# Optimization experiments

Hardware: AMD Instinct MI355X
Metric: run time of the kernel (lower is better)

Reference implementation:

```python
import jax, jax.numpy as jnp
import numpy as np

B, H, W, C = 16, 64, 64, 192
NUM_HEADS, KEY_DIM, KS = 8, 32, 3


def setup_inputs() -> dict:
    key = jax.random.key(0)
    ks = jax.random.split(key, 9)
    Ck = C + 2  # key/value input dim: patches concat 2 dist channels
    def w(k, shape, fan_in):
        return jax.random.normal(k, shape, jnp.float32) / np.float32(np.sqrt(fan_in))
    return {
        "x": jax.random.normal(ks[0], (B, H, W, C), jnp.float32),
        "Wq": w(ks[1], (C, NUM_HEADS, KEY_DIM), C),
        "bq": jnp.zeros((NUM_HEADS, KEY_DIM), jnp.float32),
        "Wk": w(ks[2], (Ck, NUM_HEADS, KEY_DIM), Ck),
        "bk": jnp.zeros((NUM_HEADS, KEY_DIM), jnp.float32),
        "Wv": w(ks[3], (Ck, NUM_HEADS, KEY_DIM), Ck),
        "bv": jnp.zeros((NUM_HEADS, KEY_DIM), jnp.float32),
        "Wo": w(ks[4], (NUM_HEADS, KEY_DIM, C), NUM_HEADS * KEY_DIM),
        "bo": jnp.zeros((C,), jnp.float32),
    }


def _local_window_kv(x, ks):
    # tf.image.extract_patches SAME (zero pad) -> [B,H,W,ks*ks,C]
    pad = ks // 2
    xp = jnp.pad(x, ((0, 0), (pad, pad), (pad, pad), (0, 0)))
    b, h, w, c = x.shape
    patches = jnp.stack(
        [xp[:, i:i + h, j:j + w, :] for i in range(ks) for j in range(ks)], axis=3
    )  # [B,H,W,ks*ks,C], row-major over window like extract_patches
    # relative distances: tf.meshgrid default 'xy', concat (dists[0], dists[1])
    r = jnp.arange(ks, dtype=x.dtype) - ks // 2
    dx, dy = jnp.meshgrid(r, r)  # 'xy' indexing, matches tf.meshgrid default
    dists = jnp.stack([dx, dy], axis=-1).reshape(ks * ks, 2)  # [9,2]
    dists = jnp.broadcast_to(dists, (b, h, w, ks * ks, 2))
    return jnp.concatenate([patches, dists], axis=-1)  # [B,H,W,9,C+2]


def reference(x, Wq, bq, Wk, bk, Wv, bv, Wo, bo):
    kv_in = _local_window_kv(x, KS)  # [B,H,W,9,C+2]
    # keras MultiHeadAttention projections
    q = jnp.einsum('bxyc,chd->bxyhd', x, Wq) + bq           # [B,H,W,h,d] (q_len=1)
    k = jnp.einsum('bxykc,chd->bxykhd', kv_in, Wk) + bk     # [B,H,W,9,h,d]
    v = jnp.einsum('bxykc,chd->bxykhd', kv_in, Wv) + bv
    scale = np.float32(1.0 / np.sqrt(KEY_DIM))
    scores = jnp.einsum('bxyhd,bxykhd->bxyhk', q, k) * scale  # [B,H,W,h,9]
    attn = jax.nn.softmax(scores, axis=-1)
    o = jnp.einsum('bxyhk,bxykhd->bxyhd', attn, v)
    return jnp.einsum('bxyhd,hdc->bxyc', o, Wo) + bo          # [B,H,W,C]
```

## Files before the change

kernel.cpp:

```cpp
#include <hip/hip_runtime.h>
#include <hip/hip_bf16.h>


typedef __bf16 bf16x8_t __attribute__((ext_vector_type(8)));
typedef float f32x4_t __attribute__((ext_vector_type(4)));

#define SCALE 0.17677669529663687f
#define QSTRIDE 864
#define ZROW 65536

static __device__ __forceinline__ unsigned short bfbits(float f) {
    return __builtin_bit_cast(unsigned short, __float2bfloat16(f));
}
static __device__ __forceinline__ float bf2f(unsigned short u) {
    return __bfloat162float(__builtin_bit_cast(__hip_bfloat16, u));
}
static __device__ __forceinline__ float lo16f(unsigned int u) {
    return __builtin_bit_cast(float, u << 16);
}
static __device__ __forceinline__ float hi16f(unsigned int u) {
    return __builtin_bit_cast(float, u & 0xffff0000u);
}

static __device__ __forceinline__ void gload_lds16(const void* g, void* l) {
    __builtin_amdgcn_global_load_lds((const __attribute__((address_space(1))) void*)g,
                                     (__attribute__((address_space(3))) void*)l, 16, 0, 0);
}

__global__ void k_convert_x(const float* __restrict__ x, ushort4* __restrict__ xb, int n4) {
    int i = blockIdx.x * blockDim.x + threadIdx.x;
    const int stride = gridDim.x * blockDim.x;
    const float4* x4 = reinterpret_cast<const float4*>(x);
    for (; i < n4; i += stride) {
        float4 v = x4[i];
        ushort4 o;
        o.x = bfbits(v.x); o.y = bfbits(v.y); o.z = bfbits(v.z); o.w = bfbits(v.w);
        xb[i] = o;
    }
}

__global__ void k_pack(const float* __restrict__ Wq, const float* __restrict__ Wk,
                       const float* __restrict__ Wv, const float* __restrict__ Wo,
                       const float* __restrict__ bq, const float* __restrict__ bk,
                       const float* __restrict__ bv,
                       __hip_bfloat16* __restrict__ WqkvT, __hip_bfloat16* __restrict__ WoT,
                       float* __restrict__ qkvBias, float* __restrict__ wvTab,
                       __hip_bfloat16* __restrict__ QKV) {
    const int idx = blockIdx.x * blockDim.x + threadIdx.x;
    const int T0 = 896 * 192;
    const int T1 = T0 + 192 * 256;
    const int T2 = T1 + 896;
    const int T3 = T2 + 768;
    const int T4 = T3 + QSTRIDE;
    if (idx < T0) {
        const int m = idx / 192, k = idx % 192;
        float v = 0.f;
        if (m < 256) {
            v = Wq[k * 256 + m] * SCALE;
        } else if (m < 768) {
            const int j = m - 256, g = j >> 3, r = j & 7;
            const int d = 4 * g + (r & 3);
            v = (r < 4) ? Wk[k * 256 + d] : Wv[k * 256 + d];
        } else if (m < 864) {
            const int j = m - 768, h = j / 12, n = j % 12;
            if (n < 9) {
                const float dj = (float)(n % 3 - 1), di = (float)(n / 3 - 1);
                float acc = 0.f;
                for (int d = 0; d < 32; ++d) {
                    const int c = h * 32 + d;
                    const float bkv = dj * Wk[192 * 256 + c] + di * Wk[193 * 256 + c] + bk[c];
                    acc += Wq[k * 256 + c] * bkv;
                }
                v = acc * SCALE;
            }
        }
        WqkvT[m * 192 + k] = __float2bfloat16(v);
    } else if (idx < T1) {
        const int j = idx - T0;
        const int c = j >> 8, hd = j & 255;
        WoT[j] = __float2bfloat16(Wo[hd * 192 + c]);
    } else if (idx < T2) {
        const int col = idx - T1;
        float v = 0.f;
        if (col < 256) v = bq[col] * SCALE;
        else if (col >= 768 && col < 864) {
            const int j = col - 768, h = j / 12, n = j % 12;
            if (n < 9) {
                const float dj = (float)(n % 3 - 1), di = (float)(n / 3 - 1);
                float acc = 0.f;
                for (int d = 0; d < 32; ++d) {
                    const int c = h * 32 + d;
                    const float bkv = dj * Wk[192 * 256 + c] + di * Wk[193 * 256 + c] + bk[c];
                    acc += bq[c] * bkv;
                }
                v = acc * SCALE;
            }
        }
        qkvBias[col] = v;
    } else if (idx < T3) {
        const int j = idx - T2;
        const int t = j >> 8, m = j & 255;
        float v;
        if (t == 0)      v = Wv[192 * 256 + m];
        else if (t == 1) v = Wv[193 * 256 + m];
        else             v = bv[m];
        wvTab[j] = v;
    } else if (idx < T4) {
        const int j = idx - T3;
        QKV[(size_t)ZROW * QSTRIDE + j] = __float2bfloat16(0.f);
    }
}

template<int BM, int BN, int WRN, int WCN, int KDIM, int NOUT, int NBX, bool OUTF32, bool BIAS>
__global__ __launch_bounds__(256) void k_gemm_lds(const __hip_bfloat16* __restrict__ A,
                          const __hip_bfloat16* __restrict__ BT,
                          void* __restrict__ Cout,
                          const float* __restrict__ bias, int ldc) {
    constexpr int WTR = BM / WRN;
    constexpr int WTC = BN / WCN;
    constexpr int FR = WTR / 16;
    constexpr int FC = WTC / 16;
    constexpr int NK = KDIM / 64;
    __shared__ __hip_bfloat16 sA[BM * 64];
    __shared__ __hip_bfloat16 sB[BN * 64];
    const int bid = blockIdx.x;
    const int s = (bid & 7) * ((int)gridDim.x >> 3) + (bid >> 3);
    const int by = s / NBX, bx = s - by * NBX;
    const int tid = threadIdx.x;
    const int wave = tid >> 6, lane = tid & 63;
    const int wr = wave / WCN, wc = wave % WCN;
    const long rowBase = (long)by * BM;
    const long colBase = (long)bx * BN;
    const int lr = lane & 15, lk = lane >> 4;
    const int srow = lane >> 3;
    const int scol = (lane & 7) * 8;

    f32x4_t acc[FR][FC] = {};
    for (int t = 0; t < NK; ++t) {
        const int k0 = t * 64;
        #pragma unroll
        for (int r = 0; r < BM / 32; ++r) {
            const int row0 = r * 32 + wave * 8;
            gload_lds16(A + (rowBase + row0 + srow) * KDIM + k0 + scol, sA + row0 * 64);
        }
        #pragma unroll
        for (int r = 0; r < BN / 32; ++r) {
            const int row0 = r * 32 + wave * 8;
            gload_lds16(BT + (colBase + row0 + srow) * KDIM + k0 + scol, sB + row0 * 64);
        }
        __syncthreads();
        #pragma unroll
        for (int kk = 0; kk < 64; kk += 32) {
            bf16x8_t a[FR], b[FC];
            #pragma unroll
            for (int fr = 0; fr < FR; ++fr)
                a[fr] = *reinterpret_cast<const bf16x8_t*>(sA + (wr * WTR + fr * 16 + lr) * 64 + kk + lk * 8);
            #pragma unroll
            for (int fc = 0; fc < FC; ++fc)
                b[fc] = *reinterpret_cast<const bf16x8_t*>(sB + (wc * WTC + fc * 16 + lr) * 64 + kk + lk * 8);
            #pragma unroll
            for (int fr = 0; fr < FR; ++fr) {
                #pragma unroll
                for (int fc = 0; fc < FC; ++fc)
                    acc[fr][fc] = __builtin_amdgcn_mfma_f32_16x16x32_bf16(a[fr], b[fc], acc[fr][fc], 0, 0, 0);
            }
        }
        __syncthreads();
    }
    const int rowSub = (lane >> 4) * 4;
    const int colSub = lane & 15;
    #pragma unroll
    for (int fr = 0; fr < FR; ++fr) {
        #pragma unroll
        for (int fc = 0; fc < FC; ++fc) {
            const long col = colBase + wc * WTC + fc * 16 + colSub;
            if (col >= NOUT) continue;
            float bvv = BIAS ? bias[col] : 0.f;
            #pragma unroll
            for (int r = 0; r < 4; ++r) {
                const long row = rowBase + wr * WTR + fr * 16 + rowSub + r;
                float v = acc[fr][fc][r] + bvv;
                if constexpr (OUTF32) ((float*)Cout)[row * ldc + col] = v;
                else ((__hip_bfloat16*)Cout)[row * ldc + col] = __float2bfloat16(v);
            }
        }
    }
}

__global__ __launch_bounds__(256) void k_attn(const __hip_bfloat16* __restrict__ QKV,
                       const float* __restrict__ wvTab,
                       __hip_bfloat16* __restrict__ O) {
    const int wave = threadIdx.x >> 6;
    const int lane = threadIdx.x & 63;
    const int bid = blockIdx.x;
    const int sblk = (bid & 7) * 2048 + (bid >> 3);
    const int p = sblk * 4 + wave;
    const int y = (p >> 6) & 63;
    const int xq = p & 63;
    const int h = lane >> 3, dg = lane & 7;
    const int idx = h * 32 + dg * 4;
    const __hip_bfloat16* rowQ = QKV + (size_t)p * QSTRIDE;

    const ushort4 qu = *reinterpret_cast<const ushort4*>(rowQ + idx);
    const float q0 = bf2f(qu.x), q1 = bf2f(qu.y), q2 = bf2f(qu.z), q3 = bf2f(qu.w);

    const ushort4 qba = *reinterpret_cast<const ushort4*>(rowQ + 768 + 12 * h);
    const ushort4 qbb = *reinterpret_cast<const ushort4*>(rowQ + 772 + 12 * h);
    const unsigned short qbc = *reinterpret_cast<const unsigned short*>(rowQ + 776 + 12 * h);
    float qb[9] = { bf2f(qba.x), bf2f(qba.y), bf2f(qba.z), bf2f(qba.w),
                    bf2f(qbb.x), bf2f(qbb.y), bf2f(qbb.z), bf2f(qbb.w), bf2f(qbc) };

    const char* baseQ = reinterpret_cast<const char*>(QKV);
    const long rowByte = (long)p * (QSTRIDE * 2);
    const int laneOff = 512 + 128 * h + 16 * dg;
    uint4 kv[9];
    #pragma unroll
    for (int n = 0; n < 9; ++n) {
        const int di = n / 3 - 1, dj = n % 3 - 1;
        const int ny = y + di, nx = xq + dj;
        const bool inb = ((unsigned)ny < 64u) & ((unsigned)nx < 64u);
        const long off = inb ? rowByte + (long)((di * 64 + dj) * (QSTRIDE * 2))
                             : (long)ZROW * (QSTRIDE * 2);
        kv[n] = *reinterpret_cast<const uint4*>(baseQ + off + laneOff);
    }

    float sc[9];
    #pragma unroll
    for (int n = 0; n < 9; ++n) {
        const float k0 = lo16f(kv[n].x), k1 = hi16f(kv[n].x);
        const float k2 = lo16f(kv[n].y), k3 = hi16f(kv[n].y);
        float ss = fmaf(q0, k0, fmaf(q1, k1, fmaf(q2, k2, q3 * k3)));
        ss += __shfl_xor(ss, 1);
        ss += __shfl_xor(ss, 2);
        ss += __shfl_xor(ss, 4);
        sc[n] = ss + qb[n];
    }
    float mx = sc[0];
    #pragma unroll
    for (int n = 1; n < 9; ++n) mx = fmaxf(mx, sc[n]);
    float sum = 0.f;
    #pragma unroll
    for (int n = 0; n < 9; ++n) { sc[n] = __expf(sc[n] - mx); sum += sc[n]; }
    const float inv = 1.0f / sum;
    const float Ej = (sc[2] + sc[5] + sc[8]) - (sc[0] + sc[3] + sc[6]);
    const float Ei = (sc[6] + sc[7] + sc[8]) - (sc[0] + sc[1] + sc[2]);

    float o0 = 0.f, o1 = 0.f, o2 = 0.f, o3 = 0.f;
    #pragma unroll
    for (int n = 0; n < 9; ++n) {
        o0 = fmaf(sc[n], lo16f(kv[n].z), o0);
        o1 = fmaf(sc[n], hi16f(kv[n].z), o1);
        o2 = fmaf(sc[n], lo16f(kv[n].w), o2);
        o3 = fmaf(sc[n], hi16f(kv[n].w), o3);
    }
    const float4 w0 = *reinterpret_cast<const float4*>(wvTab + idx);
    const float4 w1 = *reinterpret_cast<const float4*>(wvTab + 256 + idx);
    const float4 w2 = *reinterpret_cast<const float4*>(wvTab + 512 + idx);
    o0 = fmaf(Ej, w0.x, fmaf(Ei, w1.x, o0)) * inv + w2.x;
    o1 = fmaf(Ej, w0.y, fmaf(Ei, w1.y, o1)) * inv + w2.y;
    o2 = fmaf(Ej, w0.z, fmaf(Ei, w1.z, o2)) * inv + w2.z;
    o3 = fmaf(Ej, w0.w, fmaf(Ei, w1.w, o3)) * inv + w2.w;

    ushort4 ov;
    ov.x = bfbits(o0); ov.y = bfbits(o1); ov.z = bfbits(o2); ov.w = bfbits(o3);
    *reinterpret_cast<ushort4*>(O + (size_t)p * 256 + idx) = ov;
}

extern "C" void kernel_launch(void* const* d_in, const int* in_sizes, int n_in,
                              void* d_out, int out_size, void* d_ws, size_t ws_size,
                              hipStream_t stream) {
    (void)in_sizes; (void)n_in; (void)out_size; (void)ws_size;
    const float* x  = (const float*)d_in[0];
    const float* Wq = (const float*)d_in[1];
    const float* bq = (const float*)d_in[2];
    const float* Wk = (const float*)d_in[3];
    const float* bk = (const float*)d_in[4];
    const float* Wv = (const float*)d_in[5];
    const float* bv = (const float*)d_in[6];
    const float* Wo = (const float*)d_in[7];
    const float* bo = (const float*)d_in[8];

    char* ws = (char*)d_ws;
    __hip_bfloat16* xb    = (__hip_bfloat16*)(ws + 0);
    __hip_bfloat16* O     = (__hip_bfloat16*)(ws + 0);
    __hip_bfloat16* QKV   = (__hip_bfloat16*)(ws + 33554432);
    __hip_bfloat16* WqkvT = (__hip_bfloat16*)(ws + 146802368);
    __hip_bfloat16* WoT   = (__hip_bfloat16*)(ws + 147146432);
    float* qkvBias        = (float*)(ws + 147244736);
    float* wvTab          = (float*)(ws + 147248320);

    k_convert_x<<<4096, 256, 0, stream>>>(x, (ushort4*)xb, 12582912 / 4);
    k_pack<<<874, 256, 0, stream>>>(Wq, Wk, Wv, Wo, bq, bk, bv, WqkvT, WoT, qkvBias, wvTab, QKV);
    k_gemm_lds<128, 128, 2, 2, 192, 864, 7, false, true>
        <<<3584, 256, 0, stream>>>(xb, WqkvT, (void*)QKV, qkvBias, QSTRIDE);
    k_attn<<<16384, 256, 0, stream>>>(QKV, wvTab, O);
    k_gemm_lds<128, 64, 2, 2, 256, 192, 3, true, true>
        <<<1536, 256, 0, stream>>>(O, WoT, d_out, bo, 192);
}
```

Baseline: 120.1 us.

## Keep full B tile resident in LDS and read A directly from global

The GEMM kernel now stages the whole K-extent of the weight tile into LDS once, with an XOR swizzle to avoid bank conflicts, and drops the per-k-step A staging. Each wave reads its A fragments directly from global memory into registers. This removes the per-iteration barriers and LDS round-trips for A. In exchange, A reuse across the waves that share rows now depends on the cache, global A loads are uncoalesced 16-byte fragment reads, and the larger LDS footprint may lower occupancy.

```diff
diff --git a/kernel.cpp b/kernel.cpp
--- a/kernel.cpp
+++ b/kernel.cpp
@@ -112,7 +112,7 @@
 }
 
 template<int BM, int BN, int WRN, int WCN, int KDIM, int NOUT, int NBX, bool OUTF32, bool BIAS>
-__global__ __launch_bounds__(256) void k_gemm_lds(const __hip_bfloat16* __restrict__ A,
+__global__ __launch_bounds__(256) void k_gemm_bres(const __hip_bfloat16* __restrict__ A,
                           const __hip_bfloat16* __restrict__ BT,
                           void* __restrict__ Cout,
                           const float* __restrict__ bias, int ldc) {
@@ -120,53 +120,49 @@
     constexpr int WTC = BN / WCN;
     constexpr int FR = WTR / 16;
     constexpr int FC = WTC / 16;
-    constexpr int NK = KDIM / 64;
-    __shared__ __hip_bfloat16 sA[BM * 64];
-    __shared__ __hip_bfloat16 sB[BN * 64];
+    constexpr int CH = KDIM / 8;
+    constexpr int NSTG = BN * CH / 256;
+    __shared__ __hip_bfloat16 sB[BN * KDIM];
     const int bid = blockIdx.x;
     const int s = (bid & 7) * ((int)gridDim.x >> 3) + (bid >> 3);
     const int by = s / NBX, bx = s - by * NBX;
     const int tid = threadIdx.x;
     const int wave = tid >> 6, lane = tid & 63;
     const int wr = wave / WCN, wc = wave % WCN;
-    const long rowBase = (long)by * BM;
+    const long rowBase = (long)by * BM + wr * WTR;
     const long colBase = (long)bx * BN;
     const int lr = lane & 15, lk = lane >> 4;
-    const int srow = lane >> 3;
-    const int scol = (lane & 7) * 8;
+
+    #pragma unroll
+    for (int r = 0; r < NSTG; ++r) {
+        const int g = r * 256 + tid;
+        const int row = g / CH, p = g % CH;
+        const int l = p ^ (row & 7);
+        gload_lds16(BT + (colBase + row) * KDIM + l * 8, sB + g * 8);
+    }
+    __syncthreads();
 
     f32x4_t acc[FR][FC] = {};
-    for (int t = 0; t < NK; ++t) {
-        const int k0 = t * 64;
-        #pragma unroll
-        for (int r = 0; r < BM / 32; ++r) {
-            const int row0 = r * 32 + wave * 8;
-            gload_lds16(A + (rowBase + row0 + srow) * KDIM + k0 + scol, sA + row0 * 64);
-        }
-        #pragma unroll
-        for (int r = 0; r < BN / 32; ++r) {
-            const int row0 = r * 32 + wave * 8;
-            gload_lds16(BT + (colBase + row0 + srow) * KDIM + k0 + scol, sB + row0 * 64);
-        }
-        __syncthreads();
-        #pragma unroll
-        for (int kk = 0; kk < 64; kk += 32) {
-            bf16x8_t a[FR], b[FC];
-            #pragma unroll
-            for (int fr = 0; fr < FR; ++fr)
-                a[fr] = *reinterpret_cast<const bf16x8_t*>(sA + (wr * WTR + fr * 16 + lr) * 64 + kk + lk * 8);
+    #pragma unroll
+    for (int k0 = 0; k0 < KDIM; k0 += 32) {
+        bf16x8_t a[FR], b[FC];
+        #pragma unroll
+        for (int fr = 0; fr < FR; ++fr)
+            a[fr] = *reinterpret_cast<const bf16x8_t*>(A + (rowBase + fr * 16 + lr) * KDIM + k0 + lk * 8);
+        #pragma unroll
+        for (int fc = 0; fc < FC; ++fc) {
+            const int col = wc * WTC + fc * 16 + lr;
+            const int p = ((k0 / 8) + lk) ^ (col & 7);
+            b[fc] = *reinterpret_cast<const bf16x8_t*>(sB + col * KDIM + p * 8);
+        }
+        #pragma unroll
+        for (int fr = 0; fr < FR; ++fr) {
             #pragma unroll
             for (int fc = 0; fc < FC; ++fc)
-                b[fc] = *reinterpret_cast<const bf16x8_t*>(sB + (wc * WTC + fc * 16 + lr) * 64 + kk + lk * 8);
-            #pragma unroll
-            for (int fr = 0; fr < FR; ++fr) {
-                #pragma unroll
-                for (int fc = 0; fc < FC; ++fc)
-                    acc[fr][fc] = __builtin_amdgcn_mfma_f32_16x16x32_bf16(a[fr], b[fc], acc[fr][fc], 0, 0, 0);
-            }
-        }
-        __syncthreads();
-    }
+                acc[fr][fc] = __builtin_amdgcn_mfma_f32_16x16x32_bf16(a[fr], b[fc], acc[fr][fc], 0, 0, 0);
+        }
+    }
+
     const int rowSub = (lane >> 4) * 4;
     const int colSub = lane & 15;
     #pragma unroll
@@ -178,7 +174,7 @@
             float bvv = BIAS ? bias[col] : 0.f;
             #pragma unroll
             for (int r = 0; r < 4; ++r) {
-                const long row = rowBase + wr * WTR + fr * 16 + rowSub + r;
+                const long row = rowBase + fr * 16 + rowSub + r;
                 float v = acc[fr][fc][r] + bvv;
                 if constexpr (OUTF32) ((float*)Cout)[row * ldc + col] = v;
                 else ((__hip_bfloat16*)Cout)[row * ldc + col] = __float2bfloat16(v);
@@ -291,9 +287,9 @@
 
     k_convert_x<<<4096, 256, 0, stream>>>(x, (ushort4*)xb, 12582912 / 4);
     k_pack<<<874, 256, 0, stream>>>(Wq, Wk, Wv, Wo, bq, bk, bv, WqkvT, WoT, qkvBias, wvTab, QKV);
-    k_gemm_lds<128, 128, 2, 2, 192, 864, 7, false, true>
+    k_gemm_bres<128, 128, 2, 2, 192, 864, 7, false, true>
         <<<3584, 256, 0, stream>>>(xb, WqkvT, (void*)QKV, qkvBias, QSTRIDE);
     k_attn<<<16384, 256, 0, stream>>>(QKV, wvTab, O);
-    k_gemm_lds<128, 64, 2, 2, 256, 192, 3, true, true>
+    k_gemm_bres<128, 64, 2, 2, 256, 192, 3, true, true>
         <<<1536, 256, 0, stream>>>(O, WoT, d_out, bo, 192);
 }
```

Result: slower. 154.3 us (+28.4%).

## Fuse fp32-to-bf16 conversion into QKV GEMM and pipeline with swizzled LDS

Applied to the files above, without the earlier changes.

The standalone x conversion kernel is removed. The QKV GEMM now loads fp32 x through registers, converts it to bf16 and writes it into LDS itself. The GEMM also gains a double-buffered B tile (prefetched via global_load_lds for the next k-step) and XOR-swizzled LDS layouts for both A and B to avoid bank conflicts. The intent is to remove a full read/write pass over x and to overlap loads with MFMA work, at the cost of more registers and extra barriers for the register-staged A path. Each QKV block now reads fp32 A directly, so x is re-read in its 4-byte form once per column block.

```diff
diff --git a/kernel.cpp b/kernel.cpp
--- a/kernel.cpp
+++ b/kernel.cpp
@@ -25,18 +25,6 @@
 static __device__ __forceinline__ void gload_lds16(const void* g, void* l) {
     __builtin_amdgcn_global_load_lds((const __attribute__((address_space(1))) void*)g,
                                      (__attribute__((address_space(3))) void*)l, 16, 0, 0);
-}
-
-__global__ void k_convert_x(const float* __restrict__ x, ushort4* __restrict__ xb, int n4) {
-    int i = blockIdx.x * blockDim.x + threadIdx.x;
-    const int stride = gridDim.x * blockDim.x;
-    const float4* x4 = reinterpret_cast<const float4*>(x);
-    for (; i < n4; i += stride) {
-        float4 v = x4[i];
-        ushort4 o;
-        o.x = bfbits(v.x); o.y = bfbits(v.y); o.z = bfbits(v.z); o.w = bfbits(v.w);
-        xb[i] = o;
-    }
 }
 
 __global__ void k_pack(const float* __restrict__ Wq, const float* __restrict__ Wk,
@@ -111,8 +99,9 @@
     }
 }
 
-template<int BM, int BN, int WRN, int WCN, int KDIM, int NOUT, int NBX, bool OUTF32, bool BIAS>
-__global__ __launch_bounds__(256) void k_gemm_lds(const __hip_bfloat16* __restrict__ A,
+template<int BM, int BN, int WRN, int WCN, int KDIM, int NOUT, int NBX,
+         bool AF32, bool OUTF32, bool BIAS>
+__global__ __launch_bounds__(256) void k_gemm(const void* __restrict__ Ain,
                           const __hip_bfloat16* __restrict__ BT,
                           void* __restrict__ Cout,
                           const float* __restrict__ bias, int ldc) {
@@ -121,8 +110,9 @@
     constexpr int FR = WTR / 16;
     constexpr int FC = WTC / 16;
     constexpr int NK = KDIM / 64;
+    constexpr int AR = BM / 32;
     __shared__ __hip_bfloat16 sA[BM * 64];
-    __shared__ __hip_bfloat16 sB[BN * 64];
+    __shared__ __hip_bfloat16 sB[2][BN * 64];
     const int bid = blockIdx.x;
     const int s = (bid & 7) * ((int)gridDim.x >> 3) + (bid >> 3);
     const int by = s / NBX, bx = s - by * NBX;
@@ -132,32 +122,83 @@
     const long rowBase = (long)by * BM;
     const long colBase = (long)bx * BN;
     const int lr = lane & 15, lk = lane >> 4;
+    const int rx = lr & 7;
     const int srow = lane >> 3;
-    const int scol = (lane & 7) * 8;
-
-    f32x4_t acc[FR][FC] = {};
-    for (int t = 0; t < NK; ++t) {
-        const int k0 = t * 64;
-        #pragma unroll
-        for (int r = 0; r < BM / 32; ++r) {
-            const int row0 = r * 32 + wave * 8;
-            gload_lds16(A + (rowBase + row0 + srow) * KDIM + k0 + scol, sA + row0 * 64);
-        }
+    const int scolsw = ((lane & 7) ^ srow) * 8;
+    const int arow = tid >> 3;
+    const int ac = tid & 7;
+    const int apc = (ac ^ (arow & 7)) * 8;
+
+    const float* Af = (const float*)Ain;
+    const __hip_bfloat16* Ab = (const __hip_bfloat16*)Ain;
+
+    float4 f[AR][2];
+    uint4 u[AR];
+
+    auto loadA = [&](int t) {
+        #pragma unroll
+        for (int rr = 0; rr < AR; ++rr) {
+            const long row = rowBase + rr * 32 + arow;
+            if constexpr (AF32) {
+                const float* p = Af + row * KDIM + t * 64 + ac * 8;
+                f[rr][0] = *reinterpret_cast<const float4*>(p);
+                f[rr][1] = *reinterpret_cast<const float4*>(p + 4);
+            } else {
+                u[rr] = *reinterpret_cast<const uint4*>(Ab + row * KDIM + t * 64 + ac * 8);
+            }
+        }
+    };
+    auto writeA = [&]() {
+        #pragma unroll
+        for (int rr = 0; rr < AR; ++rr) {
+            const int row = rr * 32 + arow;
+            uint4 w;
+            if constexpr (AF32) {
+                w.x = (unsigned)bfbits(f[rr][0].x) | ((unsigned)bfbits(f[rr][0].y) << 16);
+                w.y = (unsigned)bfbits(f[rr][0].z) | ((unsigned)bfbits(f[rr][0].w) << 16);
+                w.z = (unsigned)bfbits(f[rr][1].x) | ((unsigned)bfbits(f[rr][1].y) << 16);
+                w.w = (unsigned)bfbits(f[rr][1].z) | ((unsigned)bfbits(f[rr][1].w) << 16);
+            } else {
+                w = u[rr];
+            }
+            *reinterpret_cast<uint4*>(&sA[row * 64 + apc]) = w;
+        }
+    };
+    auto stageB = [&](int buf, int t) {
         #pragma unroll
         for (int r = 0; r < BN / 32; ++r) {
             const int row0 = r * 32 + wave * 8;
-            gload_lds16(BT + (colBase + row0 + srow) * KDIM + k0 + scol, sB + row0 * 64);
-        }
-        __syncthreads();
-        #pragma unroll
-        for (int kk = 0; kk < 64; kk += 32) {
+            gload_lds16(BT + (colBase + row0 + srow) * KDIM + t * 64 + scolsw,
+                        &sB[buf][row0 * 64]);
+        }
+    };
+
+    f32x4_t acc[FR][FC] = {};
+
+    loadA(0);
+    stageB(0, 0);
+    writeA();
+    __syncthreads();
+
+    #pragma unroll
+    for (int t = 0; t < NK; ++t) {
+        if (t + 1 < NK) {
+            loadA(t + 1);
+            stageB((t + 1) & 1, t + 1);
+        }
+        #pragma unroll
+        for (int kk = 0; kk < 2; ++kk) {
             bf16x8_t a[FR], b[FC];
             #pragma unroll
-            for (int fr = 0; fr < FR; ++fr)
-                a[fr] = *reinterpret_cast<const bf16x8_t*>(sA + (wr * WTR + fr * 16 + lr) * 64 + kk + lk * 8);
+            for (int fr = 0; fr < FR; ++fr) {
+                const int row = wr * WTR + fr * 16 + lr;
+                a[fr] = *reinterpret_cast<const bf16x8_t*>(&sA[row * 64 + ((lk + kk * 4) ^ rx) * 8]);
+            }
             #pragma unroll
-            for (int fc = 0; fc < FC; ++fc)
-                b[fc] = *reinterpret_cast<const bf16x8_t*>(sB + (wc * WTC + fc * 16 + lr) * 64 + kk + lk * 8);
+            for (int fc = 0; fc < FC; ++fc) {
+                const int col = wc * WTC + fc * 16 + lr;
+                b[fc] = *reinterpret_cast<const bf16x8_t*>(&sB[t & 1][col * 64 + ((lk + kk * 4) ^ rx) * 8]);
+            }
             #pragma unroll
             for (int fr = 0; fr < FR; ++fr) {
                 #pragma unroll
@@ -165,8 +206,13 @@
                     acc[fr][fc] = __builtin_amdgcn_mfma_f32_16x16x32_bf16(a[fr], b[fc], acc[fr][fc], 0, 0, 0);
             }
         }
-        __syncthreads();
-    }
+        if (t + 1 < NK) {
+            __syncthreads();
+            writeA();
+            __syncthreads();
+        }
+    }
+
     const int rowSub = (lane >> 4) * 4;
     const int colSub = lane & 15;
     #pragma unroll
@@ -281,7 +327,6 @@
     const float* bo = (const float*)d_in[8];
 
     char* ws = (char*)d_ws;
-    __hip_bfloat16* xb    = (__hip_bfloat16*)(ws + 0);
     __hip_bfloat16* O     = (__hip_bfloat16*)(ws + 0);
     __hip_bfloat16* QKV   = (__hip_bfloat16*)(ws + 33554432);
     __hip_bfloat16* WqkvT = (__hip_bfloat16*)(ws + 146802368);
@@ -289,11 +334,10 @@
     float* qkvBias        = (float*)(ws + 147244736);
     float* wvTab          = (float*)(ws + 147248320);
 
-    k_convert_x<<<4096, 256, 0, stream>>>(x, (ushort4*)xb, 12582912 / 4);
     k_pack<<<874, 256, 0, stream>>>(Wq, Wk, Wv, Wo, bq, bk, bv, WqkvT, WoT, qkvBias, wvTab, QKV);
-    k_gemm_lds<128, 128, 2, 2, 192, 864, 7, false, true>
-        <<<3584, 256, 0, stream>>>(xb, WqkvT, (void*)QKV, qkvBias, QSTRIDE);
+    k_gemm<128, 128, 2, 2, 192, 864, 7, true, false, true>
+        <<<3584, 256, 0, stream>>>(x, WqkvT, (void*)QKV, qkvBias, QSTRIDE);
     k_attn<<<16384, 256, 0, stream>>>(QKV, wvTab, O);
-    k_gemm_lds<128, 64, 2, 2, 256, 192, 3, true, true>
+    k_gemm<128, 64, 2, 2, 256, 192, 3, false, true, true>
         <<<1536, 256, 0, stream>>>(O, WoT, d_out, bo, 192);
 }
```

Result: no change. 120.7 us (+0.5%).
